# Performance work log

Hardware: AMD Instinct MI355X
Metric: run time of the kernel (lower is better)

## Reference

```python
import jax, jax.numpy as jnp
import numpy as np

NPG = 32          # nodes per graph
G = 2048          # number of graphs
V = G * NPG       # 65536 nodes
DEG = 4           # incoming edges per node
E = V * DEG       # 262144 edges
H = 200           # hidden feat size
NODE_IN = 74
EDGE_IN = 12
N_LAYERS = 5
T = 2             # readout GRU timesteps


def setup_inputs() -> dict:
    key = jax.random.key(0)
    ks = jax.random.split(key, 24)

    def p(k, shape, s=0.1):
        return jax.random.normal(k, shape, jnp.float32) * s

    node_feat = jax.random.normal(ks[0], (V, NODE_IN), jnp.float32)
    edge_feat = jax.random.normal(ks[1], (E, EDGE_IN), jnp.float32)
    # graph structure: each node gets DEG incoming edges from random nodes of the same graph
    dst = jnp.repeat(jnp.arange(V, dtype=jnp.int32), DEG)
    src = (dst // NPG) * NPG + jax.random.randint(ks[2], (E,), 0, NPG, dtype=jnp.int32)
    graph_id = jnp.arange(V, dtype=jnp.int32) // NPG

    return dict(
        node_feat=node_feat, edge_feat=edge_feat, src=src, dst=dst, graph_id=graph_id,
        node_W=p(ks[3], (NODE_IN, H)), node_b=p(ks[4], (H,)),
        edge_W=p(ks[5], (EDGE_IN, H)), edge_b=p(ks[6], (H,)),
        gnn_W=p(ks[7], (N_LAYERS, H, H)), gnn_b=p(ks[8], (N_LAYERS, H)),
        lg_W=p(ks[9], (T, 2 * H, 1)), lg_b=p(ks[10], (T, 1)),
        pr_W=p(ks[11], (T, H, H)), pr_b=p(ks[12], (T, H)),
        W_ih=p(ks[13], (T, 3 * H, H)), W_hh=p(ks[14], (T, 3 * H, H)),
        b_ih=p(ks[15], (T, 3 * H)), b_hh=p(ks[16], (T, 3 * H)),
    )


def reference(node_feat, edge_feat, src, dst, graph_id,
              node_W, node_b, edge_W, edge_b, gnn_W, gnn_b,
              lg_W, lg_b, pr_W, pr_b, W_ih, W_hh, b_ih, b_hh):
    # embedding (dropout layers are identity at eval)
    h = node_feat @ node_W + node_b        # [V, H]
    eh = edge_feat @ edge_W + edge_b       # [E, H]

    # GCN layers with edge features, aggr == 'no_relu'
    for i in range(N_LAYERS):
        m = h[src] + eh                                              # u_add_e, [E, H]
        mx = jax.ops.segment_max(m, dst, num_segments=V)             # edge_softmax over incoming edges
        ex = jnp.exp(m - mx[dst])
        den = jax.ops.segment_sum(ex, dst, num_segments=V)
        a = ex / den[dst]
        agg = jax.ops.segment_sum(m * a, dst, num_segments=V)        # [V, H]
        h = jax.nn.relu(agg @ gnn_W[i] + gnn_b[i]) + h               # mlp + relu + residual

    # AttentiveFP readout
    gf = jax.ops.segment_sum(h, graph_id, num_segments=G)            # [G, H]
    for t in range(T):
        zin = jnp.concatenate([jax.nn.relu(gf)[graph_id], h], axis=1)  # [V, 2H]
        z = jax.nn.leaky_relu(zin @ lg_W[t] + lg_b[t])                  # [V, 1]
        zmax = jax.ops.segment_max(z, graph_id, num_segments=G)        # softmax_nodes
        e = jnp.exp(z - zmax[graph_id])
        a = e / jax.ops.segment_sum(e, graph_id, num_segments=G)[graph_id]
        hv = h @ pr_W[t] + pr_b[t]
        ctx = jax.nn.elu(jax.ops.segment_sum(hv * a, graph_id, num_segments=G))  # [G, H]
        # torch GRUCell: gates ordered (r, z, n)
        gi = ctx @ W_ih[t].T + b_ih[t]
        gh = gf @ W_hh[t].T + b_hh[t]
        ir, iz, inn = jnp.split(gi, 3, axis=1)
        hr, hz, hn = jnp.split(gh, 3, axis=1)
        r = jax.nn.sigmoid(ir + hr)
        u = jax.nn.sigmoid(iz + hz)
        n = jnp.tanh(inn + r * hn)
        gf = (1.0 - u) * n + u * gf
    return gf
```

## Files before the change

kernel.cpp:

```cpp
#include <hip/hip_runtime.h>
#include <hip/hip_bf16.h>
#include <math.h>

#define V 65536
#define G 2048
#define NPG 32
#define DEG 4
#define NE (V*DEG)
#define H 200
#define NODE_IN 74
#define EDGE_IN 12
#define NL 5

#define KP 224
#define NP 208
#define AGSC 101
#define EK 32
#define HS 200

typedef __attribute__((ext_vector_type(8))) short short8;
typedef __attribute__((ext_vector_type(4))) float floatx4;
typedef __attribute__((ext_vector_type(2))) float float2v;

__device__ __forceinline__ float sigmoidf_(float x) { return 1.f / (1.f + __expf(-x)); }

__device__ __forceinline__ unsigned f2bf_bits(float f) {
    unsigned u = __float_as_uint(f);
    return (u + 0x7fffu + ((u >> 16) & 1u)) >> 16;
}
__device__ __forceinline__ float bf2f(unsigned bits) { return __uint_as_float(bits << 16); }
__device__ __forceinline__ unsigned lo_bits(float f, unsigned hb) {
    return f2bf_bits(f - bf2f(hb));
}

#define EFB (NE / 256)
#define SEG_W (NL * NP * KP)
#define SEG_EW NP
#define WBLOCKS ((SEG_W + SEG_EW + 255) / 256)
#define EMBB (V / 16)
__global__ __launch_bounds__(256) void k_prep_embed(const float* __restrict__ ef,
                                                    const float* __restrict__ gnnW,
                                                    const float* __restrict__ eW,
                                                    const float* __restrict__ eb,
                                                    const float* __restrict__ nf,
                                                    const float* __restrict__ nW,
                                                    const float* __restrict__ nb,
                                                    unsigned short* __restrict__ Aedge,
                                                    unsigned short* __restrict__ WtHi,
                                                    unsigned short* __restrict__ WtLo,
                                                    unsigned short* __restrict__ eWp,
                                                    float* __restrict__ h) {
    __shared__ float smem[256 * EDGE_IN];
    const int tid = threadIdx.x, blk = blockIdx.x;

    if (blk >= EFB + WBLOCKS) {
        float (*fs)[NODE_IN] = (float (*)[NODE_IN])smem;
        const int base = (blk - EFB - WBLOCKS) * 16;
        for (int p = tid; p < 16 * NODE_IN; p += 256) {
            int n = p / NODE_IN, i = p - n * NODE_IN;
            fs[n][i] = nf[(base + n) * NODE_IN + i];
        }
        __syncthreads();
        const int j = tid;
        if (j < H) {
            float acc[16];
#pragma unroll
            for (int n = 0; n < 16; n++) acc[n] = 0.f;
            for (int i = 0; i < NODE_IN; i++) {
                float w = nW[i * H + j];
#pragma unroll
                for (int n = 0; n < 16; n++) acc[n] = fmaf(fs[n][i], w, acc[n]);
            }
            float bj = nb[j];
            for (int n = 0; n < 16; n++) h[(base + n) * H + j] = acc[n] + bj;
        }
        return;
    }

    if (blk < EFB) {
        float* efs = smem;
        const float4* gs = (const float4*)(ef + (size_t)blk * 256 * EDGE_IN);
        float4* ds = (float4*)efs;
        for (int p = tid; p < 256 * EDGE_IN / 4; p += 256) ds[p] = gs[p];
        __syncthreads();
        unsigned hb[EDGE_IN], lb[EDGE_IN];
        for (int k = 0; k < EDGE_IN; k++) {
            float v = efs[tid * EDGE_IN + k];
            hb[k] = f2bf_bits(v);
            lb[k] = lo_bits(v, hb[k]);
        }
        unsigned w[16];
        for (int i = 0; i < 6; i++) w[i] = hb[2 * i] | (hb[2 * i + 1] << 16);
        for (int i = 0; i < 6; i++) w[6 + i] = lb[2 * i] | (lb[2 * i + 1] << 16);
        w[12] = 0x3F803F80u;
        w[13] = 0u; w[14] = 0u; w[15] = 0u;
        uint4* dst = (uint4*)(Aedge + ((size_t)blk * 256 + tid) * EK);
        dst[0] = make_uint4(w[0], w[1], w[2], w[3]);
        dst[1] = make_uint4(w[4], w[5], w[6], w[7]);
        dst[2] = make_uint4(w[8], w[9], w[10], w[11]);
        dst[3] = make_uint4(w[12], w[13], w[14], w[15]);
        return;
    }
    int idx = (blk - EFB) * 256 + tid;
    if (idx < SEG_W) {
        int l = idx / (NP * KP);
        int rem = idx - l * (NP * KP);
        int n = rem / KP;
        int k = rem - n * KP;
        float w = (n < H && k < H) ? gnnW[l * H * H + k * H + n] : 0.f;
        unsigned hb = f2bf_bits(w);
        WtHi[idx] = (unsigned short)hb;
        WtLo[idx] = (unsigned short)lo_bits(w, hb);
        return;
    }
    idx -= SEG_W;
    if (idx < SEG_EW) {
        int t = idx;
        unsigned short row[64];
        for (int i = 0; i < 64; i++) row[i] = 0;
        if (t < H) {
            for (int k = 0; k < EDGE_IN; k++) {
                float w = eW[k * H + t];
                unsigned hb = f2bf_bits(w);
                row[k] = (unsigned short)hb;
                row[12 + k] = (unsigned short)hb;
                row[32 + k] = (unsigned short)lo_bits(w, hb);
            }
            float e = eb[t];
            unsigned ebh = f2bf_bits(e);
            row[24] = (unsigned short)ebh;
            row[25] = (unsigned short)lo_bits(e, ebh);
        }
        for (int i = 0; i < 64; i++) eWp[t * 64 + i] = row[i];
    }
}

__global__ __launch_bounds__(256, 4) void k_mega(float* __restrict__ h,
                                                 const unsigned short* __restrict__ Aedge,
                                                 const unsigned short* __restrict__ eWp,
                                                 const int* __restrict__ src,
                                                 const unsigned short* __restrict__ WtHi,
                                                 const unsigned short* __restrict__ WtLo,
                                                 const float* __restrict__ gnn_b,
                                                 float* __restrict__ gf_out,
                                                 const float* __restrict__ lgW,
                                                 const float* __restrict__ lgb,
                                                 float* __restrict__ wh_out) {
    __shared__ alignas(16) float h_s[NPG * HS];
    __shared__ alignas(16) unsigned int aggc[NPG * AGSC];
    __shared__ alignas(16) unsigned int zpad[8];
    __shared__ unsigned char src_s[NPG * DEG];
    const int g = blockIdx.x, tid = threadIdx.x;
    const int nbase = g * NPG, ebase = g * NPG * DEG;

    const int wave = tid >> 6, lane = tid & 63;
    const int l15 = lane & 15, quad = lane >> 4;
    const int ntcnt = (wave == 0) ? 4 : 3;

    const int mtA = wave * 2, mtB = mtA + 1;
    short8 afA, afB;
    {
        const unsigned short* abase = Aedge + (size_t)ebase * EK;
        afA = *(const short8*)&abase[(16 * mtA + l15) * EK + quad * 8];
        afB = *(const short8*)&abase[(16 * mtB + l15) * EK + quad * 8];
    }
    if (tid < NPG * DEG) src_s[tid] = (unsigned char)(src[ebase + tid] - nbase);
    if (tid < 8) zpad[tid] = 0u;
    {
        const float4* hsrc = (const float4*)(h + (size_t)nbase * H);
        float4* hdst = (float4*)h_s;
        for (int p = tid; p < NPG * H / 4; p += 256) hdst[p] = hsrc[p];
    }
    __syncthreads();

    const int nodeA = 4 * mtA + quad, nodeB = 4 * mtB + quad;
    int gsA[4], gsB[4];
#pragma unroll
    for (int e = 0; e < 4; e++) {
        gsA[e] = (int)src_s[nodeA * 4 + e] * HS;
        gsB[e] = (int)src_s[nodeB * 4 + e] * HS;
    }
    unsigned short* rowA = (unsigned short*)(aggc + nodeA * AGSC);
    unsigned short* rowB = (unsigned short*)(aggc + nodeB * AGSC);
    const float2v L2E2 = {1.4426950408889634f, 1.4426950408889634f};

    const int ntb0[3] = {0, 6, 10};
    const int ntb1[3] = {6, 10, 13};
    const int ksb0[3] = {0, 3, 5};
    const int ksb1[3] = {3, 5, 7};

    for (int l = 0; l < NL; l++) {
        floatx4 acc2[2][4];
#pragma unroll
        for (int mt = 0; mt < 2; mt++)
#pragma unroll
            for (int i = 0; i < 4; i++) acc2[mt][i] = (floatx4){0.f, 0.f, 0.f, 0.f};

        const unsigned short* WH = WtHi + (size_t)l * NP * KP;
        const unsigned short* WL = WtLo + (size_t)l * NP * KP;

        for (int ch = 0; ch < 3; ch++) {
            const int nt0 = ntb0[ch], nt1 = ntb1[ch];
            const int ks0 = ksb0[ch], ks1 = ksb1[ch];

            for (int nt = nt0; nt < nt1; nt++) {
                const int jj = nt * 16 + l15;
                const int jloc = jj - nt0 * 16;
                const int jc = jj < H ? jj : H - 1;
                const int colo = (jloc >> 3) * 16 + (jloc & 7);
                const bool val = (jj < H);
                short8 b1 = *(const short8*)&eWp[(size_t)jj * 64 + quad * 8];
                short8 b2 = *(const short8*)&eWp[(size_t)jj * 64 + 32 + quad * 8];

                auto unit = [&](short8 af, const int* gs, unsigned short* rowp) {
                    floatx4 z = (floatx4){0.f, 0.f, 0.f, 0.f};
                    z = __builtin_amdgcn_mfma_f32_16x16x32_bf16(af, b1, z, 0, 0, 0);
                    z = __builtin_amdgcn_mfma_f32_16x16x32_bf16(af, b2, z, 0, 0, 0);
                    floatx4 mh4;
#pragma unroll
                    for (int e = 0; e < 4; e++) mh4[e] = h_s[gs[e] + jc];
                    float2v mlo = __builtin_shufflevector(z, z, 0, 1) +
                                  __builtin_shufflevector(mh4, mh4, 0, 1);
                    float2v mhi = __builtin_shufflevector(z, z, 2, 3) +
                                  __builtin_shufflevector(mh4, mh4, 2, 3);
                    float mx = fmaxf(fmaxf(mlo[0], mlo[1]), fmaxf(mhi[0], mhi[1]));
                    float nm = -mx * 1.4426950408889634f;
                    float2v nm2 = {nm, nm};
                    float2v dlo = mlo * L2E2 + nm2;
                    float2v dhi = mhi * L2E2 + nm2;
                    floatx4 ev;
                    ev[0] = __builtin_amdgcn_exp2f(dlo[0]);
                    ev[1] = __builtin_amdgcn_exp2f(dlo[1]);
                    ev[2] = __builtin_amdgcn_exp2f(dhi[0]);
                    ev[3] = __builtin_amdgcn_exp2f(dhi[1]);
                    float2v elo = __builtin_shufflevector(ev, ev, 0, 1);
                    float2v ehi = __builtin_shufflevector(ev, ev, 2, 3);
                    float2v dsum = elo + ehi;
                    float2v nsum = mlo * elo + mhi * ehi;
                    float den = dsum[0] + dsum[1];
                    float num = nsum[0] + nsum[1];
                    float a = __fdividef(num, den);
                    if (!val) a = 0.f;
                    __bf16 bh = (__bf16)a;
                    float r = a - (float)bh;
                    __bf16 bl = (__bf16)r;
                    rowp[colo] = __builtin_bit_cast(unsigned short, bh);
                    rowp[colo + 8] = __builtin_bit_cast(unsigned short, bl);
                };
                unit(afA, gsA, rowA);
                unit(afB, gsB, rowB);
            }
            __syncthreads();

            for (int ks = ks0; ks < ks1; ks++) {
                const int c = 4 * ks + quad;
                const int cl = c - 4 * ks0;
                short8 ah[2], al[2];
#pragma unroll
                for (int mt = 0; mt < 2; mt++) {
                    const unsigned int* ap = (c < 26) ? &aggc[(16 * mt + l15) * AGSC + cl * 8]
                                                      : (const unsigned int*)zpad;
                    ah[mt] = *(const short8*)ap;
                    al[mt] = *(const short8*)(ap + 4);
                }
#pragma unroll 4
                for (int i = 0; i < ntcnt; i++) {
                    int nt = wave + 4 * i;
                    size_t boff = (size_t)(16 * nt + l15) * KP + ks * 32 + quad * 8;
                    short8 vbh = *(const short8*)&WH[boff];
                    short8 vbl = *(const short8*)&WL[boff];
#pragma unroll
                    for (int mt = 0; mt < 2; mt++) {
                        acc2[mt][i] = __builtin_amdgcn_mfma_f32_16x16x32_bf16(ah[mt], vbh, acc2[mt][i], 0, 0, 0);
                        acc2[mt][i] = __builtin_amdgcn_mfma_f32_16x16x32_bf16(al[mt], vbh, acc2[mt][i], 0, 0, 0);
                        acc2[mt][i] = __builtin_amdgcn_mfma_f32_16x16x32_bf16(ah[mt], vbl, acc2[mt][i], 0, 0, 0);
                    }
                }
            }

            if (ch == 2) {
                for (int i = 0; i < ntcnt; i++) {
                    int nt = wave + 4 * i, jj = nt * 16 + l15;
                    if (jj < H) {
                        float bj = gnn_b[l * H + jj];
#pragma unroll
                        for (int mt = 0; mt < 2; mt++) {
#pragma unroll
                            for (int r = 0; r < 4; r++) {
                                float v = acc2[mt][i][r] + bj;
                                v = v > 0.f ? v : 0.f;
                                h_s[(16 * mt + quad * 4 + r) * HS + jj] += v;
                            }
                        }
                    }
                }
            }
            __syncthreads();
        }
    }

    {
        float4* dst = (float4*)(h + (size_t)nbase * H);
        const float4* srcp = (const float4*)h_s;
        for (int p = tid; p < NPG * H / 4; p += 256) dst[p] = srcp[p];
    }
    float* gf_s = (float*)aggc;
    float* z_s = gf_s + 224;
    float* a_s = gf_s + 256;
    float* den_p = gf_s + 288;
    if (tid < H) {
        float s = 0.f;
        for (int n = 0; n < NPG; n++) s += h_s[n * HS + tid];
        gf_out[g * H + tid] = s;
        gf_s[tid] = s;
    }
    __syncthreads();
    {
        const int n = tid >> 3, l8 = tid & 7;
        float p = 0.f;
        for (int jj = l8; jj < H; jj += 8) {
            p = fmaf(h_s[n * HS + jj], lgW[H + jj], p);
            p = fmaf(fmaxf(gf_s[jj], 0.f), lgW[jj], p);
        }
        p += __shfl_xor(p, 1);
        p += __shfl_xor(p, 2);
        p += __shfl_xor(p, 4);
        if (l8 == 0) {
            float z = p + lgb[0];
            z_s[n] = z > 0.f ? z : 0.01f * z;
        }
    }
    __syncthreads();
    if (tid < 64) {
        float z = (lane < NPG) ? z_s[lane] : -1e30f;
        float m = z;
        m = fmaxf(m, __shfl_xor(m, 1));
        m = fmaxf(m, __shfl_xor(m, 2));
        m = fmaxf(m, __shfl_xor(m, 4));
        m = fmaxf(m, __shfl_xor(m, 8));
        m = fmaxf(m, __shfl_xor(m, 16));
        float e = (lane < NPG) ? __expf(z - m) : 0.f;
        float d = e;
        d += __shfl_xor(d, 1);
        d += __shfl_xor(d, 2);
        d += __shfl_xor(d, 4);
        d += __shfl_xor(d, 8);
        d += __shfl_xor(d, 16);
        if (lane < NPG) a_s[lane] = e;
        if (lane == 0) den_p[0] = d;
    }
    __syncthreads();
    if (tid < H) {
        float s = 0.f;
        for (int n = 0; n < NPG; n++) s = fmaf(a_s[n], h_s[n * HS + tid], s);
        wh_out[g * H + tid] = s / den_p[0];
    }
}

__global__ __launch_bounds__(256) void k_attn(const float* __restrict__ h,
                                              const float* __restrict__ gf,
                                              const float* __restrict__ lgW,
                                              const float* __restrict__ lgb,
                                              float* __restrict__ wh_out) {
    __shared__ float h_s[NPG][H];
    __shared__ float gf_s[H];
    __shared__ float z_s[NPG];
    __shared__ float a_s[NPG];
    __shared__ float den_s;
    const int g = blockIdx.x, tid = threadIdx.x;
    const int lane = tid & 63;

    for (int p = tid; p < NPG * H; p += 256) h_s[0][p] = h[g * NPG * H + p];
    if (tid < H) gf_s[tid] = gf[g * H + tid];
    __syncthreads();

    {
        const int n = tid >> 3, l = tid & 7;
        float p = 0.f;
        for (int jj = l; jj < H; jj += 8) {
            p = fmaf(h_s[n][jj], lgW[H + jj], p);
            p = fmaf(fmaxf(gf_s[jj], 0.f), lgW[jj], p);
        }
        p += __shfl_xor(p, 1);
        p += __shfl_xor(p, 2);
        p += __shfl_xor(p, 4);
        if (l == 0) {
            float z = p + lgb[0];
            z_s[n] = z > 0.f ? z : 0.01f * z;
        }
    }
    __syncthreads();

    if (tid < 64) {
        float z = (lane < NPG) ? z_s[lane] : -1e30f;
        float m = z;
        m = fmaxf(m, __shfl_xor(m, 1));
        m = fmaxf(m, __shfl_xor(m, 2));
        m = fmaxf(m, __shfl_xor(m, 4));
        m = fmaxf(m, __shfl_xor(m, 8));
        m = fmaxf(m, __shfl_xor(m, 16));
        float e = (lane < NPG) ? __expf(z - m) : 0.f;
        float d = e;
        d += __shfl_xor(d, 1);
        d += __shfl_xor(d, 2);
        d += __shfl_xor(d, 4);
        d += __shfl_xor(d, 8);
        d += __shfl_xor(d, 16);
        if (lane < NPG) a_s[lane] = e;
        if (lane == 0) den_s = d;
    }
    __syncthreads();

    if (tid < H) {
        float s = 0.f;
        for (int n = 0; n < NPG; n++) s = fmaf(a_s[n], h_s[n][tid], s);
        wh_out[g * H + tid] = s / den_s;
    }
}

#define GPB 8
#define GP 9
__global__ __launch_bounds__(512) void k_projgru(const float* __restrict__ wh,
                                                 const float* __restrict__ gf,
                                                 const float* __restrict__ prW,
                                                 const float* __restrict__ prb,
                                                 const float* __restrict__ Wih,
                                                 const float* __restrict__ Whh,
                                                 const float* __restrict__ bih,
                                                 const float* __restrict__ bhh,
                                                 float* __restrict__ gf_out) {
    __shared__ float wh_s[GPB][H];
    __shared__ float gfs[GPB][H];
    __shared__ float ctx_s[GPB][H];
    __shared__ float gi_s[3 * H][GP];
    __shared__ float gh_s[3 * H][GP];
    const int gbase = blockIdx.x * GPB, tid = threadIdx.x;

    for (int p = tid; p < GPB * H; p += 512) {
        wh_s[0][p] = wh[(size_t)gbase * H + p];
        gfs[0][p] = gf[(size_t)gbase * H + p];
    }
    __syncthreads();

    {
        const int j = tid;
        if (j < H) {
            float acc[GPB];
#pragma unroll
            for (int q = 0; q < GPB; q++) acc[q] = 0.f;
            for (int i = 0; i < H; i++) {
                float w = prW[i * H + j];
#pragma unroll
                for (int q = 0; q < GPB; q++) acc[q] = fmaf(wh_s[q][i], w, acc[q]);
            }
            float bj = prb[j];
            for (int q = 0; q < GPB; q++) {
                float s = acc[q] + bj;
                ctx_s[q][j] = s > 0.f ? s : __expf(s) - 1.f;
            }
        }
    }
    __syncthreads();

    for (int k = tid; k < 3 * H; k += 512) {
        float ai[GPB], ah[GPB];
        float bi = bih[k], bh = bhh[k];
#pragma unroll
        for (int q = 0; q < GPB; q++) { ai[q] = bi; ah[q] = bh; }
        const float4* wi4 = (const float4*)(Wih + (size_t)k * H);
        const float4* wh4 = (const float4*)(Whh + (size_t)k * H);
        for (int j4 = 0; j4 < H / 4; j4++) {
            float4 wi = wi4[j4];
            float4 wg = wh4[j4];
            int jj = j4 * 4;
#pragma unroll
            for (int q = 0; q < GPB; q++) {
                ai[q] = fmaf(ctx_s[q][jj + 0], wi.x, ai[q]);
                ai[q] = fmaf(ctx_s[q][jj + 1], wi.y, ai[q]);
                ai[q] = fmaf(ctx_s[q][jj + 2], wi.z, ai[q]);
                ai[q] = fmaf(ctx_s[q][jj + 3], wi.w, ai[q]);
                ah[q] = fmaf(gfs[q][jj + 0], wg.x, ah[q]);
                ah[q] = fmaf(gfs[q][jj + 1], wg.y, ah[q]);
                ah[q] = fmaf(gfs[q][jj + 2], wg.z, ah[q]);
                ah[q] = fmaf(gfs[q][jj + 3], wg.w, ah[q]);
            }
        }
#pragma unroll
        for (int q = 0; q < GPB; q++) { gi_s[k][q] = ai[q]; gh_s[k][q] = ah[q]; }
    }
    __syncthreads();

    for (int p = tid; p < GPB * H; p += 512) {
        int q = p / H, jj = p - q * H;
        float r = sigmoidf_(gi_s[jj][q] + gh_s[jj][q]);
        float u = sigmoidf_(gi_s[H + jj][q] + gh_s[H + jj][q]);
        float nn = tanhf(gi_s[2 * H + jj][q] + r * gh_s[2 * H + jj][q]);
        gf_out[(gbase + q) * H + jj] = (1.f - u) * nn + u * gfs[q][jj];
    }
}

extern "C" void kernel_launch(void* const* d_in, const int* in_sizes, int n_in,
                              void* d_out, int out_size, void* d_ws, size_t ws_size,
                              hipStream_t stream) {
    const float* node_feat = (const float*)d_in[0];
    const float* edge_feat = (const float*)d_in[1];
    const int* src = (const int*)d_in[2];
    const float* node_W = (const float*)d_in[5];
    const float* node_b = (const float*)d_in[6];
    const float* edge_W = (const float*)d_in[7];
    const float* edge_b = (const float*)d_in[8];
    const float* gnn_W = (const float*)d_in[9];
    const float* gnn_b = (const float*)d_in[10];
    const float* lg_W = (const float*)d_in[11];
    const float* lg_b = (const float*)d_in[12];
    const float* pr_W = (const float*)d_in[13];
    const float* pr_b = (const float*)d_in[14];
    const float* W_ih = (const float*)d_in[15];
    const float* W_hh = (const float*)d_in[16];
    const float* b_ih = (const float*)d_in[17];
    const float* b_hh = (const float*)d_in[18];
    float* out = (float*)d_out;

    char* ws = (char*)d_ws;
    size_t off = 0;
    auto alloc = [&](size_t bytes) { void* p = ws + off; off += (bytes + 4095) & ~(size_t)4095; return p; };
    float* h = (float*)alloc((size_t)V * H * 4);
    unsigned short* Aedge = (unsigned short*)alloc((size_t)NE * EK * 2);
    unsigned short* WtHi = (unsigned short*)alloc((size_t)NL * NP * KP * 2);
    unsigned short* WtLo = (unsigned short*)alloc((size_t)NL * NP * KP * 2);
    unsigned short* eWp = (unsigned short*)alloc((size_t)NP * 64 * 2);
    float* gf_ws = (float*)alloc((size_t)G * H * 4);
    float* wh_ws = (float*)alloc((size_t)G * H * 4);

    k_prep_embed<<<EFB + WBLOCKS + EMBB, 256, 0, stream>>>(
        edge_feat, gnn_W, edge_W, edge_b, node_feat, node_W, node_b,
        Aedge, WtHi, WtLo, eWp, h);

    k_mega<<<G, 256, 0, stream>>>(h, Aedge, eWp, src, WtHi, WtLo, gnn_b, gf_ws,
                                  lg_W, lg_b, wh_ws);

    k_projgru<<<G / GPB, 512, 0, stream>>>(wh_ws, gf_ws, pr_W, pr_b,
                                           W_ih, W_hh, b_ih, b_hh, gf_ws);
    k_attn<<<G, 256, 0, stream>>>(h, gf_ws, lg_W + 2 * H, lg_b + 1, wh_ws);
    k_projgru<<<G / GPB, 512, 0, stream>>>(wh_ws, gf_ws, pr_W + (size_t)H * H,
                                           pr_b + H,
                                           W_ih + (size_t)3 * H * H,
                                           W_hh + (size_t)3 * H * H,
                                           b_ih + 3 * H,
                                           b_hh + 3 * H, out);
}
```

Measured before the change: 643.1 us.

## Transpose and interleave GRU weights for coalesced loads in projection-GRU kernel

Adds a kernel that transposes W_ih and W_hh into an interleaved [j][k][ih/hh] layout stored in the no-longer-needed edge buffer, so adjacent threads in the GRU gate matmul read consecutive addresses instead of each thread striding through its own weight row. The projection and gate loops are also restructured so each thread computes two output columns and reads activations from shared memory as float4. This adds one transpose launch and reuses the Aedge workspace after k_mega, which depends on stream ordering. Fewer active threads per block may reduce latency hiding.

```diff
diff --git a/kernel.cpp b/kernel.cpp
--- a/kernel.cpp
+++ b/kernel.cpp
@@ -357,6 +357,24 @@
     }
 }
 
+#define SEG_T (2 * 2 * 3 * H * H)
+#define TBLOCKS ((SEG_T + 255) / 256)
+__global__ __launch_bounds__(256) void k_wgt(const float* __restrict__ W_ih,
+                                             const float* __restrict__ W_hh,
+                                             float* __restrict__ WgT) {
+    int idx = blockIdx.x * 256 + threadIdx.x;
+    if (idx < SEG_T) {
+        int tt = idx / (2 * 3 * H * H);
+        int r = idx - tt * (2 * 3 * H * H);
+        int j = r / (6 * H);
+        int r2 = r - j * (6 * H);
+        int k = r2 >> 1;
+        int m = r2 & 1;
+        const float* srcm = (m ? W_hh : W_ih) + (size_t)tt * 3 * H * H;
+        WgT[idx] = srcm[k * H + j];
+    }
+}
+
 __global__ __launch_bounds__(256) void k_attn(const float* __restrict__ h,
                                               const float* __restrict__ gf,
                                               const float* __restrict__ lgW,
@@ -424,8 +442,7 @@
                                                  const float* __restrict__ gf,
                                                  const float* __restrict__ prW,
                                                  const float* __restrict__ prb,
-                                                 const float* __restrict__ Wih,
-                                                 const float* __restrict__ Whh,
+                                                 const float* __restrict__ WgTt,
                                                  const float* __restrict__ bih,
                                                  const float* __restrict__ bhh,
                                                  float* __restrict__ gf_out) {
@@ -442,51 +459,75 @@
     }
     __syncthreads();
 
-    {
+    if (tid < 100) {
         const int j = tid;
-        if (j < H) {
-            float acc[GPB];
-#pragma unroll
-            for (int q = 0; q < GPB; q++) acc[q] = 0.f;
-            for (int i = 0; i < H; i++) {
-                float w = prW[i * H + j];
-#pragma unroll
-                for (int q = 0; q < GPB; q++) acc[q] = fmaf(wh_s[q][i], w, acc[q]);
-            }
-            float bj = prb[j];
+        float a0[GPB], a1[GPB];
+#pragma unroll
+        for (int q = 0; q < GPB; q++) { a0[q] = 0.f; a1[q] = 0.f; }
+        for (int c = 0; c < H / 4; c++) {
+            const int i = c * 4;
+            float wv[GPB][4];
+#pragma unroll
             for (int q = 0; q < GPB; q++) {
-                float s = acc[q] + bj;
-                ctx_s[q][j] = s > 0.f ? s : __expf(s) - 1.f;
-            }
-        }
-    }
-    __syncthreads();
-
-    for (int k = tid; k < 3 * H; k += 512) {
-        float ai[GPB], ah[GPB];
-        float bi = bih[k], bh = bhh[k];
-#pragma unroll
-        for (int q = 0; q < GPB; q++) { ai[q] = bi; ah[q] = bh; }
-        const float4* wi4 = (const float4*)(Wih + (size_t)k * H);
-        const float4* wh4 = (const float4*)(Whh + (size_t)k * H);
-        for (int j4 = 0; j4 < H / 4; j4++) {
-            float4 wi = wi4[j4];
-            float4 wg = wh4[j4];
-            int jj = j4 * 4;
+                float4 t4 = *(const float4*)&wh_s[q][i];
+                wv[q][0] = t4.x; wv[q][1] = t4.y; wv[q][2] = t4.z; wv[q][3] = t4.w;
+            }
+#pragma unroll
+            for (int jj = 0; jj < 4; jj++) {
+                float wA = prW[(i + jj) * H + j];
+                float wB = prW[(i + jj) * H + j + 100];
+#pragma unroll
+                for (int q = 0; q < GPB; q++) {
+                    a0[q] = fmaf(wv[q][jj], wA, a0[q]);
+                    a1[q] = fmaf(wv[q][jj], wB, a1[q]);
+                }
+            }
+        }
+        float b0 = prb[j], b1 = prb[j + 100];
+#pragma unroll
+        for (int q = 0; q < GPB; q++) {
+            float s0 = a0[q] + b0;
+            float s1 = a1[q] + b1;
+            ctx_s[q][j] = s0 > 0.f ? s0 : __expf(s0) - 1.f;
+            ctx_s[q][j + 100] = s1 > 0.f ? s1 : __expf(s1) - 1.f;
+        }
+    }
+    __syncthreads();
+
+    if (tid < 300) {
+        const int k0 = tid, k1 = tid + 300;
+        float ai0[GPB], ah0[GPB], ai1[GPB], ah1[GPB];
+        float bi0 = bih[k0], bh0 = bhh[k0], bi1 = bih[k1], bh1 = bhh[k1];
+#pragma unroll
+        for (int q = 0; q < GPB; q++) { ai0[q] = bi0; ah0[q] = bh0; ai1[q] = bi1; ah1[q] = bh1; }
+        for (int c = 0; c < H / 4; c++) {
+            const int j = c * 4;
+            float cx[GPB][4], gg[GPB][4];
 #pragma unroll
             for (int q = 0; q < GPB; q++) {
-                ai[q] = fmaf(ctx_s[q][jj + 0], wi.x, ai[q]);
-                ai[q] = fmaf(ctx_s[q][jj + 1], wi.y, ai[q]);
-                ai[q] = fmaf(ctx_s[q][jj + 2], wi.z, ai[q]);
-                ai[q] = fmaf(ctx_s[q][jj + 3], wi.w, ai[q]);
-                ah[q] = fmaf(gfs[q][jj + 0], wg.x, ah[q]);
-                ah[q] = fmaf(gfs[q][jj + 1], wg.y, ah[q]);
-                ah[q] = fmaf(gfs[q][jj + 2], wg.z, ah[q]);
-                ah[q] = fmaf(gfs[q][jj + 3], wg.w, ah[q]);
-            }
-        }
-#pragma unroll
-        for (int q = 0; q < GPB; q++) { gi_s[k][q] = ai[q]; gh_s[k][q] = ah[q]; }
+                float4 t4 = *(const float4*)&ctx_s[q][j];
+                cx[q][0] = t4.x; cx[q][1] = t4.y; cx[q][2] = t4.z; cx[q][3] = t4.w;
+                float4 g4 = *(const float4*)&gfs[q][j];
+                gg[q][0] = g4.x; gg[q][1] = g4.y; gg[q][2] = g4.z; gg[q][3] = g4.w;
+            }
+#pragma unroll
+            for (int jj = 0; jj < 4; jj++) {
+                float2 wa = *(const float2*)&WgTt[((size_t)(j + jj) * 600 + k0) * 2];
+                float2 wb = *(const float2*)&WgTt[((size_t)(j + jj) * 600 + k1) * 2];
+#pragma unroll
+                for (int q = 0; q < GPB; q++) {
+                    ai0[q] = fmaf(cx[q][jj], wa.x, ai0[q]);
+                    ah0[q] = fmaf(gg[q][jj], wa.y, ah0[q]);
+                    ai1[q] = fmaf(cx[q][jj], wb.x, ai1[q]);
+                    ah1[q] = fmaf(gg[q][jj], wb.y, ah1[q]);
+                }
+            }
+        }
+#pragma unroll
+        for (int q = 0; q < GPB; q++) {
+            gi_s[k0][q] = ai0[q]; gh_s[k0][q] = ah0[q];
+            gi_s[k1][q] = ai1[q]; gh_s[k1][q] = ah1[q];
+        }
     }
     __syncthreads();
 
@@ -531,6 +572,7 @@
     unsigned short* eWp = (unsigned short*)alloc((size_t)NP * 64 * 2);
     float* gf_ws = (float*)alloc((size_t)G * H * 4);
     float* wh_ws = (float*)alloc((size_t)G * H * 4);
+    float* WgT = (float*)Aedge;
 
     k_prep_embed<<<EFB + WBLOCKS + EMBB, 256, 0, stream>>>(
         edge_feat, gnn_W, edge_W, edge_b, node_feat, node_W, node_b,
@@ -539,13 +581,13 @@
     k_mega<<<G, 256, 0, stream>>>(h, Aedge, eWp, src, WtHi, WtLo, gnn_b, gf_ws,
                                   lg_W, lg_b, wh_ws);
 
+    k_wgt<<<TBLOCKS, 256, 0, stream>>>(W_ih, W_hh, WgT);
+
     k_projgru<<<G / GPB, 512, 0, stream>>>(wh_ws, gf_ws, pr_W, pr_b,
-                                           W_ih, W_hh, b_ih, b_hh, gf_ws);
+                                           WgT, b_ih, b_hh, gf_ws);
     k_attn<<<G, 256, 0, stream>>>(h, gf_ws, lg_W + 2 * H, lg_b + 1, wh_ws);
     k_projgru<<<G / GPB, 512, 0, stream>>>(wh_ws, gf_ws, pr_W + (size_t)H * H,
                                            pr_b + H,
-                                           W_ih + (size_t)3 * H * H,
-                                           W_hh + (size_t)3 * H * H,
-                                           b_ih + 3 * H,
-                                           b_hh + 3 * H, out);
-}
+                                           WgT + (size_t)2 * 3 * H * H,
+                                           b_ih + 3 * H, b_hh + 3 * H, out);
+}
```

Result: faster. 579.8 us (median of 2 runs) (-9.8%).
